# Optimization experiments

Measured on AMD Instinct MI355X. Metric: run time of the kernel, lower is better.

The kernel has to match this reference:

```python
import jax, jax.numpy as jnp
import numpy as np

D_MODEL, N_LEVELS, N_HEADS, N_POINTS = 256, 4, 8, 4
HEAD_DIM = D_MODEL // N_HEADS
SPATIAL = [(100, 100), (50, 50), (25, 25), (13, 13)]  # (H, W) per level
BATCH = 2


def setup_inputs() -> dict:
    key = jax.random.key(0)
    ks = jax.random.split(key, 10)
    len_in = sum(h * w for h, w in SPATIAL)
    n, lq = BATCH, len_in
    s = 0.02
    mlp = N_HEADS * N_LEVELS * N_POINTS
    starts = np.cumsum([0] + [h * w for h, w in SPATIAL])[:-1]
    return {
        "query": jax.random.normal(ks[0], (n, lq, D_MODEL), jnp.float32),
        "reference_points": jax.random.uniform(ks[1], (n, lq, N_LEVELS, 2), jnp.float32),
        "input_flatten": jax.random.normal(ks[2], (n, len_in, D_MODEL), jnp.float32),
        "input_spatial_shapes": jnp.array(SPATIAL, dtype=jnp.int32),
        "input_level_start_index": jnp.array(starts, dtype=jnp.int32),
        "Wv": jax.random.normal(ks[3], (D_MODEL, D_MODEL), jnp.float32) * s,
        "bv": jnp.zeros((D_MODEL,), jnp.float32),
        "Woff": jax.random.normal(ks[4], (D_MODEL, mlp * 2), jnp.float32) * s,
        "boff": jax.random.normal(ks[5], (mlp * 2,), jnp.float32) * s,
        "Wattn": jax.random.normal(ks[6], (D_MODEL, mlp), jnp.float32) * s,
        "battn": jnp.zeros((mlp,), jnp.float32),
        "Wout": jax.random.normal(ks[7], (D_MODEL, D_MODEL), jnp.float32) * s,
        "bout": jnp.zeros((D_MODEL,), jnp.float32),
    }


def _ms_deform_attn_core(value, spatial_shapes, loc, aw):
    """value [N,S,M,D]; loc [N,Lq,M,L,P,2] in [0,1]; aw [N,Lq,M,L,P] -> [N,Lq,M*D].
    Faithful to F.grid_sample(mode='bilinear', padding_mode='zeros', align_corners=False)."""
    n, lq, m, L, p, _ = loc.shape
    d = value.shape[-1]
    out = jnp.zeros((n, m, lq, d), value.dtype)
    gather = jax.vmap(jax.vmap(lambda v, i: v[i]))  # vmap over N and M
    start = 0
    for lvl, (H, W) in enumerate(spatial_shapes):
        v = value[:, start:start + H * W].transpose(0, 2, 1, 3)  # [N,M,HW,D]
        start += H * W
        # align_corners=False: grid g=2*loc-1 -> pixel = ((g+1)*size-1)/2 = loc*size-0.5
        x = loc[:, :, :, lvl, :, 0] * W - 0.5  # [N,Lq,M,P]
        y = loc[:, :, :, lvl, :, 1] * H - 0.5
        x0 = jnp.floor(x)
        y0 = jnp.floor(y)
        wx = x - x0
        wy = y - y0
        x0i = x0.astype(jnp.int32)
        y0i = y0.astype(jnp.int32)
        samp = jnp.zeros((n, m, lq * p, d), value.dtype)
        for dy, wyc in ((0, 1.0 - wy), (1, wy)):
            for dx, wxc in ((0, 1.0 - wx), (1, wx)):
                xi = x0i + dx
                yi = y0i + dy
                valid = (xi >= 0) & (xi < W) & (yi >= 0) & (yi < H)  # zeros padding
                idx = jnp.clip(yi, 0, H - 1) * W + jnp.clip(xi, 0, W - 1)
                idx = idx.transpose(0, 2, 1, 3).reshape(n, m, lq * p)
                w = (wxc * wyc * valid).transpose(0, 2, 1, 3).reshape(n, m, lq * p)
                samp = samp + gather(v, idx) * w[..., None]
        samp = samp.reshape(n, m, lq, p, d)
        aw_l = aw[:, :, :, lvl, :].transpose(0, 2, 1, 3)  # [N,M,Lq,P]
        out = out + (samp * aw_l[..., None]).sum(3)
    return out.transpose(0, 2, 1, 3).reshape(n, lq, m * d)


def reference(query, reference_points, input_flatten, input_spatial_shapes,
              input_level_start_index, Wv, bv, Woff, boff, Wattn, battn, Wout, bout):
    n, lq, _ = query.shape
    m, L, p = N_HEADS, N_LEVELS, N_POINTS
    shapes = np.asarray(input_spatial_shapes)  # concrete/static [L,2] = (H,W)
    value = (input_flatten @ Wv + bv).reshape(n, -1, m, HEAD_DIM)
    off = (query @ Woff + boff).reshape(n, lq, m, L, p, 2)
    aw = jax.nn.softmax((query @ Wattn + battn).reshape(n, lq, m, L * p), axis=-1)
    aw = aw.reshape(n, lq, m, L, p)
    norm = jnp.asarray(shapes[:, ::-1].astype(np.float32))  # [L,2] = (W,H)
    loc = reference_points[:, :, None, :, None, :] + off / norm[None, None, None, :, None, :]
    out = _ms_deform_attn_core(value, [tuple(s) for s in shapes.tolist()], loc, aw)
    return out @ Wout + bout
```

## Files before the change

### kernel.cpp

```cpp
#include <hip/hip_runtime.h>
#include <hip/hip_bf16.h>

#define NB    2
#define LQ    13294
#define DM    256
#define NH    8
#define HD    32
#define NL    4
#define NP    4
#define ROWS  (NB*LQ)

#define OFF_VALUE 0u
#define OFF_TMP   13613056u
#define OFF_OFFS  27226112u
#define OFF_AWL   54452224u
#define OFF_WT    61258752u
#define OFF_FLAG  61717504u

#define WT_WV    0
#define WT_WOFF  65536
#define WT_WATTN 131072
#define WT_WOUT  163840

typedef __attribute__((ext_vector_type(8))) short short8;
typedef __attribute__((ext_vector_type(4))) float floatx4;

static __device__ __forceinline__ float blo(int u)  { return __uint_as_float(((unsigned)u) << 16); }
static __device__ __forceinline__ float bhif(int u) { return __uint_as_float(((unsigned)u) & 0xffff0000u); }

static __device__ __forceinline__ int pack_bf2(float a, float b) {
    __hip_bfloat162 h(__float2bfloat16(a), __float2bfloat16(b));
    int u; __builtin_memcpy(&u, &h, 4); return u;
}

static __device__ __forceinline__ void gload_lds16(const void* g, void* l) {
    __builtin_amdgcn_global_load_lds(
        (const __attribute__((address_space(1))) unsigned*)g,
        (__attribute__((address_space(3))) unsigned*)l, 16, 0, 0);
}

__global__ void sniff_k(const unsigned int* __restrict__ q, int* __restrict__ flag) {
    const int t = threadIdx.x;
    int hits = 0;
#pragma unroll
    for (int i = 0; i < 4; ++i) {
        unsigned lo = q[t * 4 + i] & 0xffffu;
        unsigned e  = (lo >> 7) & 0xffu;
        if ((e >= 110u && e <= 132u) || lo == 0u) ++hits;
    }
#pragma unroll
    for (int s = 1; s < 64; s <<= 1) hits += __shfl_xor(hits, s);
    if (t == 0) *flag = (hits > 160) ? 1 : 0;
}

__global__ __launch_bounds__(256) void trans_k(
    const void* __restrict__ s0, const void* __restrict__ s1,
    const void* __restrict__ s2, const void* __restrict__ s3,
    short* __restrict__ wt, const int* __restrict__ flagp)
{
    const int flag = *flagp;
    const int z = blockIdx.z;
    const void* src = (z == 0) ? s0 : (z == 1) ? s1 : (z == 2) ? s2 : s3;
    short* dst = wt + ((z == 0) ? WT_WV : (z == 1) ? WT_WOFF : (z == 2) ? WT_WATTN : WT_WOUT);
    const int N = (z == 2) ? 128 : 256;
    const int n0 = blockIdx.x * 32, k0 = blockIdx.y * 32;
    if (n0 >= N) return;

    __shared__ short tile[32 * 36];
    const int t = threadIdx.x;
    const int r = t >> 3, c4 = (t & 7) * 4;
    if (flag) {
        const short* sp = (const short*)src + (k0 + r) * N + n0 + c4;
        *(short4*)&tile[r * 36 + c4] = *(const short4*)sp;
    } else {
        const float* sp = (const float*)src + (k0 + r) * N + n0 + c4;
        float4 v = *(const float4*)sp;
        short4 o;
        o.x = (short)(pack_bf2(v.x, v.x) & 0xffff);
        o.y = (short)(pack_bf2(v.y, v.y) & 0xffff);
        o.z = (short)(pack_bf2(v.z, v.z) & 0xffff);
        o.w = (short)(pack_bf2(v.w, v.w) & 0xffff);
        *(short4*)&tile[r * 36 + c4] = o;
    }
    __syncthreads();
    const int nn = t >> 3, r4 = (t & 7) * 4;
    short4 o;
    o.x = tile[(r4 + 0) * 36 + nn];
    o.y = tile[(r4 + 1) * 36 + nn];
    o.z = tile[(r4 + 2) * 36 + nn];
    o.w = tile[(r4 + 3) * 36 + nn];
    *(short4*)&dst[(n0 + nn) * 256 + k0 + r4] = o;
}

__global__ __launch_bounds__(256) void gemm_lds_k(
    const void* __restrict__ A, const short* __restrict__ Wt,
    const void* __restrict__ bias, const void* __restrict__ bias2,
    void* __restrict__ C, void* __restrict__ C2,
    int M, int Nn, int a_mode, int c_mode, const int* __restrict__ flagp)
{
    const int  flag = *flagp;
    const bool a_bf = (a_mode == 2) ? (flag != 0) : true;

    __shared__ __align__(16) short As[128 * 32];
    __shared__ __align__(16) short Bs[128 * 32];

    const int tid = threadIdx.x;
    const int w = tid >> 6, lane = tid & 63;
    const int qd = lane >> 4, ln = lane & 15;
    const int bm = blockIdx.y * 128, bn = blockIdx.x * 128;
    const int wm = (w & 1) * 64, wn = (w >> 1) * 64;

    const int ar0 = tid >> 2,        ak0 = (tid & 3) * 8;
    const int ar1 = (tid + 256) >> 2, ak1 = (tid & 3) * 8;
    const int ga0 = min(bm + ar0, M - 1), ga1 = min(bm + ar1, M - 1);
    short* lA0 = As + w * 512;
    short* lA1 = As + 2048 + w * 512;
    short* lB0 = Bs + w * 512;
    short* lB1 = Bs + 2048 + w * 512;

    floatx4 acc[4][4];
#pragma unroll
    for (int i = 0; i < 4; ++i)
#pragma unroll
        for (int j = 0; j < 4; ++j) acc[i][j] = floatx4{0.f, 0.f, 0.f, 0.f};

    const short* Ab = (const short*)A;
    const float* Af = (const float*)A;

    for (int k0 = 0; k0 < 256; k0 += 32) {
        __syncthreads();
        gload_lds16(Wt + (bn + ar0) * 256 + k0 + ak0, lB0);
        gload_lds16(Wt + (bn + ar1) * 256 + k0 + ak1, lB1);
        if (a_bf) {
            gload_lds16(Ab + ga0 * 256 + k0 + ak0, lA0);
            gload_lds16(Ab + ga1 * 256 + k0 + ak1, lA1);
        } else {
            float4 f0 = *(const float4*)(Af + ga0 * 256 + k0 + ak0);
            float4 f1 = *(const float4*)(Af + ga0 * 256 + k0 + ak0 + 4);
            int4 p0; p0.x = pack_bf2(f0.x, f0.y); p0.y = pack_bf2(f0.z, f0.w);
                     p0.z = pack_bf2(f1.x, f1.y); p0.w = pack_bf2(f1.z, f1.w);
            *(int4*)&As[ar0 * 32 + ak0] = p0;
            float4 g0 = *(const float4*)(Af + ga1 * 256 + k0 + ak1);
            float4 g1 = *(const float4*)(Af + ga1 * 256 + k0 + ak1 + 4);
            int4 p1; p1.x = pack_bf2(g0.x, g0.y); p1.y = pack_bf2(g0.z, g0.w);
                     p1.z = pack_bf2(g1.x, g1.y); p1.w = pack_bf2(g1.z, g1.w);
            *(int4*)&As[ar1 * 32 + ak1] = p1;
        }
        __syncthreads();

        short8 af[4], bf[4];
#pragma unroll
        for (int i = 0; i < 4; ++i)
            af[i] = *(const short8*)&As[(wm + i * 16 + ln) * 32 + qd * 8];
#pragma unroll
        for (int j = 0; j < 4; ++j)
            bf[j] = *(const short8*)&Bs[(wn + j * 16 + ln) * 32 + qd * 8];
#pragma unroll
        for (int i = 0; i < 4; ++i)
#pragma unroll
            for (int j = 0; j < 4; ++j)
                acc[i][j] = __builtin_amdgcn_mfma_f32_16x16x32_bf16(af[i], bf[j], acc[i][j], 0, 0, 0);
    }

#pragma unroll
    for (int j = 0; j < 4; ++j) {
        const int col = bn + wn + j * 16 + ln;
        float bj;
        if (c_mode == 3 && col >= 256) {
            if (flag) bj = __bfloat162float(((const __hip_bfloat16*)bias2)[col - 256]);
            else      bj = ((const float*)bias2)[col - 256];
        } else {
            if (flag) bj = __bfloat162float(((const __hip_bfloat16*)bias)[col]);
            else      bj = ((const float*)bias)[col];
        }
#pragma unroll
        for (int i = 0; i < 4; ++i) {
#pragma unroll
            for (int r = 0; r < 4; ++r) {
                const int row = bm + wm + i * 16 + qd * 4 + r;
                if (row >= M) continue;
                const float v = acc[i][j][r] + bj;
                if (c_mode == 0)      ((__hip_bfloat16*)C)[row * Nn + col] = __float2bfloat16(v);
                else if (c_mode == 1) ((float*)C)[row * Nn + col] = v;
                else if (c_mode == 2) {
                    if (flag) ((__hip_bfloat16*)C)[row * Nn + col] = __float2bfloat16(v);
                    else      ((float*)C)[row * Nn + col] = v;
                } else {
                    if (col < 256) ((float*)C)[row * 256 + col] = v;
                    else           ((__hip_bfloat16*)C2)[row * 128 + col - 256] = __float2bfloat16(v);
                }
            }
        }
    }
}

__global__ __launch_bounds__(256) void sampler_k(
    const void* __restrict__ refp, const short* __restrict__ value,
    const float* __restrict__ offs, const short* __restrict__ awl,
    short* __restrict__ tmp, const int* __restrict__ flagp)
{
    const int flag = *flagp;
    const int nq = blockIdx.x * 4 + (threadIdx.x >> 6);
    const int lane = threadIdx.x & 63;
    const int h = lane >> 3, u = lane & 7;
    const int n = (nq >= LQ) ? 1 : 0;

    const int lg = *(const int*)(awl + nq * 128 + h * 16 + u * 2);
    float l0 = blo(lg), l1 = bhif(lg);
    float m = fmaxf(l0, l1);
    m = fmaxf(m, __shfl_xor(m, 1));
    m = fmaxf(m, __shfl_xor(m, 2));
    m = fmaxf(m, __shfl_xor(m, 4));
    float e0 = __expf(l0 - m), e1 = __expf(l1 - m);
    float s = e0 + e1;
    s += __shfl_xor(s, 1);
    s += __shfl_xor(s, 2);
    s += __shfl_xor(s, 4);
    const float inv = 1.f / s;
    const float w0 = e0 * inv, w1 = e1 * inv;

    const float4 of = *(const float4*)(offs + nq * 256 + h * 32 + u * 4);

    float rxl, ryl;
    if (flag) {
        const int rr = *(const int*)((const short*)refp + nq * 8 + (u & 3) * 2);
        rxl = blo(rr); ryl = bhif(rr);
    } else {
        const float* rp = (const float*)refp + nq * 8 + (u & 3) * 2;
        rxl = rp[0]; ryl = rp[1];
    }

    const short* vb = value + (n ? LQ * 256 : 0) + h * 32 + u * 4;

    float a0 = 0.f, a1 = 0.f, a2 = 0.f, a3 = 0.f;

    const int WlA[NL] = {100, 50, 25, 13};
    const int StA[NL] = {0, 10000, 12500, 13125};

#pragma unroll
    for (int idx = 0; idx < 16; ++idx) {
        const int l = idx >> 2;
        const int Wl = WlA[l];
        const float Wf = (float)Wl;
        const int owner = h * 8 + (idx >> 1);
        const float ox = __shfl((idx & 1) ? of.z : of.x, owner);
        const float oy = __shfl((idx & 1) ? of.w : of.y, owner);
        const float wa = __shfl((idx & 1) ? w1 : w0, owner);
        const float rx = __shfl(rxl, h * 8 + l);
        const float ry = __shfl(ryl, h * 8 + l);

        const float px = fmaf(rx, Wf, ox) - 0.5f;
        const float py = fmaf(ry, Wf, oy) - 0.5f;
        const float x0f = floorf(px), y0f = floorf(py);
        const float wx = px - x0f, wy = py - y0f;
        const int x0 = (int)x0f, y0 = (int)y0f;
        const short* vl = vb + StA[l] * 256;

#pragma unroll
        for (int dy = 0; dy < 2; ++dy) {
#pragma unroll
            for (int dx = 0; dx < 2; ++dx) {
                const int xi = x0 + dx, yi = y0 + dy;
                const bool vld = (xi >= 0) & (xi < Wl) & (yi >= 0) & (yi < Wl);
                const float wgt = (dx ? wx : 1.f - wx) * (dy ? wy : 1.f - wy);
                const float ww = vld ? wa * wgt : 0.f;
                const int xc = min(max(xi, 0), Wl - 1);
                const int yc = min(max(yi, 0), Wl - 1);
                const int2 raw = *(const int2*)(vl + (yc * Wl + xc) * 256);
                a0 = fmaf(ww, blo(raw.x),  a0);
                a1 = fmaf(ww, bhif(raw.x), a1);
                a2 = fmaf(ww, blo(raw.y),  a2);
                a3 = fmaf(ww, bhif(raw.y), a3);
            }
        }
    }

    int2 o;
    o.x = pack_bf2(a0, a1);
    o.y = pack_bf2(a2, a3);
    *(int2*)(tmp + nq * 256 + h * 32 + u * 4) = o;
}

extern "C" void kernel_launch(void* const* d_in, const int* in_sizes, int n_in,
                              void* d_out, int out_size, void* d_ws, size_t ws_size,
                              hipStream_t stream)
{
    const void* query  = d_in[0];
    const void* refpts = d_in[1];
    const void* flat   = d_in[2];
    const void* Wv     = d_in[5];
    const void* bv     = d_in[6];
    const void* Woff   = d_in[7];
    const void* boff   = d_in[8];
    const void* Wattn  = d_in[9];
    const void* battn  = d_in[10];
    const void* Wout   = d_in[11];
    const void* bout   = d_in[12];

    char* ws = (char*)d_ws;
    short* value = (short*)(ws + OFF_VALUE);
    short* tmp   = (short*)(ws + OFF_TMP);
    float* offsb = (float*)(ws + OFF_OFFS);
    short* awl   = (short*)(ws + OFF_AWL);
    short* wt    = (short*)(ws + OFF_WT);
    int*   flagp = (int*)(ws + OFF_FLAG);

    const int gmy = (ROWS + 127) / 128;

    sniff_k<<<1, 64, 0, stream>>>((const unsigned int*)query, flagp);
    trans_k<<<dim3(8, 8, 4), 256, 0, stream>>>(Wv, Woff, Wattn, Wout, wt, flagp);
    gemm_lds_k<<<dim3(2, gmy), 256, 0, stream>>>(flat, wt + WT_WV, bv, nullptr,
                                                 value, nullptr, ROWS, 256, 2, 0, flagp);
    gemm_lds_k<<<dim3(3, gmy), 256, 0, stream>>>(query, wt + WT_WOFF, boff, battn,
                                                 offsb, awl, ROWS, 384, 2, 3, flagp);
    sampler_k<<<ROWS / 4, 256, 0, stream>>>(refpts, value, offsb, awl, tmp, flagp);
    gemm_lds_k<<<dim3(2, gmy), 256, 0, stream>>>(tmp, wt + WT_WOUT, bout, nullptr,
                                                 d_out, nullptr, ROWS, 256, 1, 2, flagp);
}
```

Before: 245.3 us.

## Fuse value and offset GEMMs into one launch with LDS-resident weight panels

Merges the value-projection and offset/attention-projection GEMMs into a single launch that picks its operand and weight by block column. Each block now loads its full-K weight panel into padded LDS once, and A fragments are read straight from global memory into registers with no per-k-step barriers. The output GEMM is reworked the same way with 64-column tiles so more blocks are launched. This removes one launch and the repeated LDS staging and syncs. In exchange each block uses much more LDS, which may lower occupancy, and A loads from global are uncoalesced fragment reads.

```diff
diff --git a/kernel.cpp b/kernel.cpp
--- a/kernel.cpp
+++ b/kernel.cpp
@@ -22,6 +22,8 @@
 #define WT_WATTN 131072
 #define WT_WOUT  163840
 
+#define BSTR 264
+
 typedef __attribute__((ext_vector_type(8))) short short8;
 typedef __attribute__((ext_vector_type(4))) float floatx4;
 
@@ -33,10 +35,20 @@
     int u; __builtin_memcpy(&u, &h, 4); return u;
 }
 
-static __device__ __forceinline__ void gload_lds16(const void* g, void* l) {
-    __builtin_amdgcn_global_load_lds(
-        (const __attribute__((address_space(1))) unsigned*)g,
-        (__attribute__((address_space(3))) unsigned*)l, 16, 0, 0);
+static __device__ __forceinline__ float load_bias(const void* b, int i, int flag) {
+    return flag ? __bfloat162float(((const __hip_bfloat16*)b)[i]) : ((const float*)b)[i];
+}
+
+static __device__ __forceinline__ short8 load_afrag(const void* A, int row, int k, bool a_bf) {
+    if (a_bf) {
+        return *(const short8*)((const short*)A + row * 256 + k);
+    } else {
+        const float* p = (const float*)A + row * 256 + k;
+        float4 f0 = *(const float4*)p, f1 = *(const float4*)(p + 4);
+        int4 pk; pk.x = pack_bf2(f0.x, f0.y); pk.y = pack_bf2(f0.z, f0.w);
+                 pk.z = pack_bf2(f1.x, f1.y); pk.w = pack_bf2(f1.z, f1.w);
+        short8 r; __builtin_memcpy(&r, &pk, 16); return r;
+    }
 }
 
 __global__ void sniff_k(const unsigned int* __restrict__ q, int* __restrict__ flag) {
@@ -92,103 +104,140 @@
     *(short4*)&dst[(n0 + nn) * 256 + k0 + r4] = o;
 }
 
-__global__ __launch_bounds__(256) void gemm_lds_k(
-    const void* __restrict__ A, const short* __restrict__ Wt,
-    const void* __restrict__ bias, const void* __restrict__ bias2,
-    void* __restrict__ C, void* __restrict__ C2,
-    int M, int Nn, int a_mode, int c_mode, const int* __restrict__ flagp)
+__global__ __launch_bounds__(256) void gemm_front_k(
+    const void* __restrict__ flat, const void* __restrict__ query,
+    const short* __restrict__ wt,
+    const void* __restrict__ bv, const void* __restrict__ boff, const void* __restrict__ battn,
+    short* __restrict__ value, float* __restrict__ offsb, short* __restrict__ awl,
+    const int* __restrict__ flagp)
 {
     const int  flag = *flagp;
-    const bool a_bf = (a_mode == 2) ? (flag != 0) : true;
-
-    __shared__ __align__(16) short As[128 * 32];
-    __shared__ __align__(16) short Bs[128 * 32];
+    const bool a_bf = (flag != 0);
+
+    __shared__ __align__(16) short Bs[128 * BSTR];
 
     const int tid = threadIdx.x;
+    const int bx = blockIdx.x;
+    const bool isv = (bx < 2);
+    const void*  A   = isv ? flat : query;
+    const short* Wtb = isv ? (wt + WT_WV) : (wt + WT_WOFF);
+    const int colbase = (isv ? bx : bx - 2) * 128;
+    const int bm = blockIdx.y * 128;
+
+#pragma unroll
+    for (int i = 0; i < 16; ++i) {
+        const int ch = i * 256 + tid;
+        const int c = ch >> 5, ks = (ch & 31) * 8;
+        *(int4*)&Bs[c * BSTR + ks] = *(const int4*)(Wtb + (colbase + c) * 256 + ks);
+    }
+    __syncthreads();
+
     const int w = tid >> 6, lane = tid & 63;
     const int qd = lane >> 4, ln = lane & 15;
-    const int bm = blockIdx.y * 128, bn = blockIdx.x * 128;
-    const int wm = (w & 1) * 64, wn = (w >> 1) * 64;
-
-    const int ar0 = tid >> 2,        ak0 = (tid & 3) * 8;
-    const int ar1 = (tid + 256) >> 2, ak1 = (tid & 3) * 8;
-    const int ga0 = min(bm + ar0, M - 1), ga1 = min(bm + ar1, M - 1);
-    short* lA0 = As + w * 512;
-    short* lA1 = As + 2048 + w * 512;
-    short* lB0 = Bs + w * 512;
-    short* lB1 = Bs + 2048 + w * 512;
-
-    floatx4 acc[4][4];
-#pragma unroll
-    for (int i = 0; i < 4; ++i)
+    const int m0 = bm + w * 32;
+    const int r0 = min(m0 + ln, ROWS - 1);
+    const int r1 = min(m0 + 16 + ln, ROWS - 1);
+
+    floatx4 acc[2][8];
+#pragma unroll
+    for (int i = 0; i < 2; ++i)
+#pragma unroll
+        for (int j = 0; j < 8; ++j) acc[i][j] = floatx4{0.f, 0.f, 0.f, 0.f};
+
+#pragma unroll
+    for (int k0 = 0; k0 < 256; k0 += 32) {
+        const int kk = k0 + qd * 8;
+        const short8 af0 = load_afrag(A, r0, kk, a_bf);
+        const short8 af1 = load_afrag(A, r1, kk, a_bf);
+#pragma unroll
+        for (int j = 0; j < 8; ++j) {
+            const short8 bf = *(const short8*)&Bs[(j * 16 + ln) * BSTR + kk];
+            acc[0][j] = __builtin_amdgcn_mfma_f32_16x16x32_bf16(af0, bf, acc[0][j], 0, 0, 0);
+            acc[1][j] = __builtin_amdgcn_mfma_f32_16x16x32_bf16(af1, bf, acc[1][j], 0, 0, 0);
+        }
+    }
+
+#pragma unroll
+    for (int j = 0; j < 8; ++j) {
+        const int col = colbase + j * 16 + ln;
+        float bj;
+        if (isv)            bj = load_bias(bv, col, flag);
+        else if (col < 256) bj = load_bias(boff, col, flag);
+        else                bj = load_bias(battn, col - 256, flag);
+#pragma unroll
+        for (int i = 0; i < 2; ++i) {
+#pragma unroll
+            for (int r = 0; r < 4; ++r) {
+                const int row = m0 + i * 16 + qd * 4 + r;
+                if (row >= ROWS) continue;
+                const float v = acc[i][j][r] + bj;
+                if (isv)            value[row * 256 + col] = (short)(pack_bf2(v, v) & 0xffff);
+                else if (col < 256) offsb[row * 256 + col] = v;
+                else                awl[row * 128 + col - 256] = (short)(pack_bf2(v, v) & 0xffff);
+            }
+        }
+    }
+}
+
+__global__ __launch_bounds__(256) void gemm_out_k(
+    const short* __restrict__ tmp, const short* __restrict__ wtout,
+    const void* __restrict__ bout, void* __restrict__ C,
+    const int* __restrict__ flagp)
+{
+    const int flag = *flagp;
+
+    __shared__ __align__(16) short Bs[64 * BSTR];
+
+    const int tid = threadIdx.x;
+    const int colbase = blockIdx.x * 64;
+    const int bm = blockIdx.y * 128;
+
+#pragma unroll
+    for (int i = 0; i < 8; ++i) {
+        const int ch = i * 256 + tid;
+        const int c = ch >> 5, ks = (ch & 31) * 8;
+        *(int4*)&Bs[c * BSTR + ks] = *(const int4*)(wtout + (colbase + c) * 256 + ks);
+    }
+    __syncthreads();
+
+    const int w = tid >> 6, lane = tid & 63;
+    const int qd = lane >> 4, ln = lane & 15;
+    const int m0 = bm + w * 32;
+    const int r0 = min(m0 + ln, ROWS - 1);
+    const int r1 = min(m0 + 16 + ln, ROWS - 1);
+
+    floatx4 acc[2][4];
+#pragma unroll
+    for (int i = 0; i < 2; ++i)
 #pragma unroll
         for (int j = 0; j < 4; ++j) acc[i][j] = floatx4{0.f, 0.f, 0.f, 0.f};
 
-    const short* Ab = (const short*)A;
-    const float* Af = (const float*)A;
-
+#pragma unroll
     for (int k0 = 0; k0 < 256; k0 += 32) {
-        __syncthreads();
-        gload_lds16(Wt + (bn + ar0) * 256 + k0 + ak0, lB0);
-        gload_lds16(Wt + (bn + ar1) * 256 + k0 + ak1, lB1);
-        if (a_bf) {
-            gload_lds16(Ab + ga0 * 256 + k0 + ak0, lA0);
-            gload_lds16(Ab + ga1 * 256 + k0 + ak1, lA1);
-        } else {
-            float4 f0 = *(const float4*)(Af + ga0 * 256 + k0 + ak0);
-            float4 f1 = *(const float4*)(Af + ga0 * 256 + k0 + ak0 + 4);
-            int4 p0; p0.x = pack_bf2(f0.x, f0.y); p0.y = pack_bf2(f0.z, f0.w);
-                     p0.z = pack_bf2(f1.x, f1.y); p0.w = pack_bf2(f1.z, f1.w);
-            *(int4*)&As[ar0 * 32 + ak0] = p0;
-            float4 g0 = *(const float4*)(Af + ga1 * 256 + k0 + ak1);
-            float4 g1 = *(const float4*)(Af + ga1 * 256 + k0 + ak1 + 4);
-            int4 p1; p1.x = pack_bf2(g0.x, g0.y); p1.y = pack_bf2(g0.z, g0.w);
-                     p1.z = pack_bf2(g1.x, g1.y); p1.w = pack_bf2(g1.z, g1.w);
-            *(int4*)&As[ar1 * 32 + ak1] = p1;
-        }
-        __syncthreads();
-
-        short8 af[4], bf[4];
-#pragma unroll
-        for (int i = 0; i < 4; ++i)
-            af[i] = *(const short8*)&As[(wm + i * 16 + ln) * 32 + qd * 8];
-#pragma unroll
-        for (int j = 0; j < 4; ++j)
-            bf[j] = *(const short8*)&Bs[(wn + j * 16 + ln) * 32 + qd * 8];
-#pragma unroll
-        for (int i = 0; i < 4; ++i)
-#pragma unroll
-            for (int j = 0; j < 4; ++j)
-                acc[i][j] = __builtin_amdgcn_mfma_f32_16x16x32_bf16(af[i], bf[j], acc[i][j], 0, 0, 0);
+        const int kk = k0 + qd * 8;
+        const short8 af0 = *(const short8*)(tmp + r0 * 256 + kk);
+        const short8 af1 = *(const short8*)(tmp + r1 * 256 + kk);
+#pragma unroll
+        for (int j = 0; j < 4; ++j) {
+            const short8 bf = *(const short8*)&Bs[(j * 16 + ln) * BSTR + kk];
+            acc[0][j] = __builtin_amdgcn_mfma_f32_16x16x32_bf16(af0, bf, acc[0][j], 0, 0, 0);
+            acc[1][j] = __builtin_amdgcn_mfma_f32_16x16x32_bf16(af1, bf, acc[1][j], 0, 0, 0);
+        }
     }
 
 #pragma unroll
     for (int j = 0; j < 4; ++j) {
-        const int col = bn + wn + j * 16 + ln;
-        float bj;
-        if (c_mode == 3 && col >= 256) {
-            if (flag) bj = __bfloat162float(((const __hip_bfloat16*)bias2)[col - 256]);
-            else      bj = ((const float*)bias2)[col - 256];
-        } else {
-            if (flag) bj = __bfloat162float(((const __hip_bfloat16*)bias)[col]);
-            else      bj = ((const float*)bias)[col];
-        }
-#pragma unroll
-        for (int i = 0; i < 4; ++i) {
+        const int col = colbase + j * 16 + ln;
+        const float bj = load_bias(bout, col, flag);
+#pragma unroll
+        for (int i = 0; i < 2; ++i) {
 #pragma unroll
             for (int r = 0; r < 4; ++r) {
-                const int row = bm + wm + i * 16 + qd * 4 + r;
-                if (row >= M) continue;
+                const int row = m0 + i * 16 + qd * 4 + r;
+                if (row >= ROWS) continue;
                 const float v = acc[i][j][r] + bj;
-                if (c_mode == 0)      ((__hip_bfloat16*)C)[row * Nn + col] = __float2bfloat16(v);
-                else if (c_mode == 1) ((float*)C)[row * Nn + col] = v;
-                else if (c_mode == 2) {
-                    if (flag) ((__hip_bfloat16*)C)[row * Nn + col] = __float2bfloat16(v);
-                    else      ((float*)C)[row * Nn + col] = v;
-                } else {
-                    if (col < 256) ((float*)C)[row * 256 + col] = v;
-                    else           ((__hip_bfloat16*)C2)[row * 128 + col - 256] = __float2bfloat16(v);
-                }
+                if (flag) ((__hip_bfloat16*)C)[row * 256 + col] = __float2bfloat16(v);
+                else      ((float*)C)[row * 256 + col] = v;
             }
         }
     }
@@ -309,11 +358,8 @@
 
     sniff_k<<<1, 64, 0, stream>>>((const unsigned int*)query, flagp);
     trans_k<<<dim3(8, 8, 4), 256, 0, stream>>>(Wv, Woff, Wattn, Wout, wt, flagp);
-    gemm_lds_k<<<dim3(2, gmy), 256, 0, stream>>>(flat, wt + WT_WV, bv, nullptr,
-                                                 value, nullptr, ROWS, 256, 2, 0, flagp);
-    gemm_lds_k<<<dim3(3, gmy), 256, 0, stream>>>(query, wt + WT_WOFF, boff, battn,
-                                                 offsb, awl, ROWS, 384, 2, 3, flagp);
+    gemm_front_k<<<dim3(5, gmy), 256, 0, stream>>>(flat, query, wt, bv, boff, battn,
+                                                   value, offsb, awl, flagp);
     sampler_k<<<ROWS / 4, 256, 0, stream>>>(refpts, value, offsb, awl, tmp, flagp);
-    gemm_lds_k<<<dim3(2, gmy), 256, 0, stream>>>(tmp, wt + WT_WOUT, bout, nullptr,
-                                                 d_out, nullptr, ROWS, 256, 1, 2, flagp);
-}
+    gemm_out_k<<<dim3(4, gmy), 256, 0, stream>>>(tmp, wt + WT_WOUT, bout, d_out, flagp);
+}
```

Result: no change. 246.8 us (+0.6%).
